# Performance work log

Hardware: AMD Instinct MI355X
Metric: run time of the kernel (lower is better)

## Reference

```python
import jax, jax.numpy as jnp
import numpy as np

B, R, NM, H, P1, G1, RC1, LAT = 16384, 360, 200, 256, 512, 256, 256, 128


def _linear_params(k, out_f, in_f):
    s = 1.0 / np.sqrt(in_f)
    kw, kb = jax.random.split(k)
    W = jax.random.uniform(kw, (out_f, in_f), minval=-s, maxval=s, dtype=jnp.float32)
    b = jax.random.uniform(kb, (out_f,), minval=-s, maxval=s, dtype=jnp.float32)
    return W, b


def setup_inputs() -> dict:
    key = jax.random.key(0)
    ks = jax.random.split(key, 14)
    x_window = jax.random.normal(ks[0], (B, 3, R), dtype=jnp.float32)
    modes = jax.random.normal(ks[1], (R, NM), dtype=jnp.float32)
    mode_coeff = jax.random.normal(ks[2], (B, NM), dtype=jnp.float32)
    W1, b1 = _linear_params(ks[3], H, 3 * R)      # surrogate layer 1
    W2, b2 = _linear_params(ks[4], H, H)          # surrogate layer 2
    W3, b3 = _linear_params(ks[5], R, H)          # surrogate layer 3
    Wp1, bp1 = _linear_params(ks[6], P1, R * R)   # npi_proj
    Wp2, bp2 = _linear_params(ks[7], LAT, P1)
    Wg1, bg1 = _linear_params(ks[8], G1, NM)      # geo_proj
    Wg2, bg2 = _linear_params(ks[9], LAT, G1)
    Wr1, br1 = _linear_params(ks[10], RC1, LAT)   # recon
    Wr2, br2 = _linear_params(ks[11], R, RC1)
    return dict(x_window=x_window, modes=modes, mode_coeff=mode_coeff,
                W1=W1, b1=b1, W2=W2, b2=b2, W3=W3, b3=b3,
                Wp1=Wp1, bp1=bp1, Wp2=Wp2, bp2=bp2,
                Wg1=Wg1, bg1=bg1, Wg2=Wg2, bg2=bg2,
                Wr1=Wr1, br1=br1, Wr2=Wr2, br2=br2)


def reference(x_window, modes, mode_coeff,
              W1, b1, W2, b2, W3, b3,
              Wp1, bp1, Wp2, bp2,
              Wg1, bg1, Wg2, bg2,
              Wr1, br1, Wr2, br2):
    Bs = x_window.shape[0]
    Rr = W3.shape[0]
    # ---- NPI surrogate forward (needed for ReLU masks) ----
    z = x_window.reshape(Bs, 3 * Rr)                       # (B, 3R)
    h1 = z @ W1.T + b1                                     # (B, H)
    m1 = (h1 > 0).astype(z.dtype)
    h2 = (h1 * m1) @ W2.T + b2                             # (B, H)
    m2 = (h2 > 0).astype(z.dtype)
    # ---- EC: exact batch-mean Jacobian of the ReLU MLP w.r.t last timestep ----
    # mean_b [ W3 diag(m2_b) W2 diag(m1_b) W1_last ] = W3 @ (W2 * (m2^T m1 / B)) @ W1[:, -R:]
    G = (m2.T @ m1) / Bs                                   # (H, H)
    ec = W3 @ ((W2 * G) @ W1[:, -Rr:])                     # (R, R); row j = dy_j/dx
    ec = jax.lax.stop_gradient(ec)                         # create_graph=False in original
    # ---- projections ----
    ec_flat = ec.reshape(1, Rr * Rr)
    z_npi1 = jax.nn.relu(ec_flat @ Wp1.T + bp1) @ Wp2.T + bp2   # (1, LAT)
    z_npi = jnp.tile(z_npi1, (Bs, 1))                           # (B, LAT)
    z_geo = jax.nn.relu(mode_coeff @ Wg1.T + bg1) @ Wg2.T + bg2  # (B, LAT)
    zsum = z_npi + z_geo
    zn = zsum / jnp.maximum(jnp.linalg.norm(zsum, axis=-1, keepdims=True), 1e-12)
    recon = jax.nn.relu(zn @ Wr1.T + br1) @ Wr2.T + br2          # (B, R)
    return (z_npi, z_geo, zn, ec, recon)
```

## Files before the change

kernel.cpp:

```cpp
#include <hip/hip_runtime.h>

typedef __bf16 bf16x8 __attribute__((ext_vector_type(8)));
typedef __bf16 bf16x4 __attribute__((ext_vector_type(4)));
typedef float  f32x4  __attribute__((ext_vector_type(4)));

__device__ __forceinline__ f32x4 mfma_bf16(bf16x8 a, bf16x8 b, f32x4 c) {
  return __builtin_amdgcn_mfma_f32_16x16x32_bf16(a, b, c, 0, 0, 0);
}
__device__ __forceinline__ bf16x8 ldB(const __bf16* Bp, int kt, int NT, int nt,
                                      int lane) {
  return *reinterpret_cast<const bf16x8*>(Bp + (((size_t)kt * NT + nt) * 64 + lane) * 8);
}

__global__ void pack_all(const float* __restrict__ W1, const float* __restrict__ W2,
                         const float* __restrict__ Wg1, const float* __restrict__ Wg2,
                         const float* __restrict__ Wr1, const float* __restrict__ Wr2,
                         __bf16* __restrict__ W1p, __bf16* __restrict__ W2p,
                         __bf16* __restrict__ Wg1p, __bf16* __restrict__ Wg2p,
                         __bf16* __restrict__ Wr1p, __bf16* __restrict__ Wr2p,
                         float* __restrict__ G) {
  int bx = blockIdx.x;
  int lane = threadIdx.x;
  if (bx >= 1104) {
    float4* g = (float4*)G;
    int base = (bx - 1104) * 512 + lane;
#pragma unroll
    for (int i = 0; i < 8; ++i) g[base + i * 64] = make_float4(0.f, 0.f, 0.f, 0.f);
    return;
  }
  const float* W; __bf16* out; int N, K, NT, local;
  if (bx < 544)      { W = W1;  out = W1p;  N = 256; K = 1080; NT = 16; local = bx; }
  else if (bx < 672) { W = W2;  out = W2p;  N = 256; K = 256;  NT = 16; local = bx - 544; }
  else if (bx < 784) { W = Wg1; out = Wg1p; N = 256; K = 200;  NT = 16; local = bx - 672; }
  else if (bx < 848) { W = Wg2; out = Wg2p; N = 128; K = 256;  NT = 8;  local = bx - 784; }
  else if (bx < 912) { W = Wr1; out = Wr1p; N = 256; K = 128;  NT = 16; local = bx - 848; }
  else               { W = Wr2; out = Wr2p; N = 360; K = 256;  NT = 24; local = bx - 912; }
  int nt = local % NT, kt = local / NT;
  int n = nt * 16 + (lane & 15);
  int k0 = kt * 32 + (lane >> 4) * 8;
  bf16x8 v;
#pragma unroll
  for (int e = 0; e < 8; ++e) {
    int k = k0 + e;
    float xv = (n < N && k < K) ? W[(size_t)n * K + k] : 0.f;
    v[e] = (__bf16)xv;
  }
  *reinterpret_cast<bf16x8*>(out + ((size_t)local * 64 + lane) * 8) = v;
}

__global__ __launch_bounds__(256) void h1h2_fused(
    const float* __restrict__ x, const __bf16* __restrict__ W1p,
    const float* __restrict__ b1, const __bf16* __restrict__ W2p,
    const float* __restrict__ b2, __bf16* __restrict__ m1T,
    __bf16* __restrict__ m2T) {
  __shared__ __bf16 Alds[32][68];
  __shared__ __bf16 h1s[32][264];
  int tid = threadIdx.x;
  int lane = tid & 63, wid = tid >> 6;
  int rowBase = blockIdx.x * 32;
  int sr = tid >> 3, sc = (tid & 7) * 8;
  const float* aSrc = x + (size_t)(rowBase + sr) * 1080;
  f32x4 acc[2][4] = {};
  float4 c0a, c0b, c1a, c1b;
  auto LD = [&](int s, float4& a, float4& b) {
    int gk = s * 64 + sc;
    if (gk < 1080) {
      a = *(const float4*)(aSrc + gk);
      b = *(const float4*)(aSrc + gk + 4);
    } else {
      a = make_float4(0.f, 0.f, 0.f, 0.f);
      b = a;
    }
  };
  LD(0, c0a, c0b);
  LD(1, c1a, c1b);
  for (int s = 0; s < 17; ++s) {
    bf16x8 w8;
    w8[0] = (__bf16)c0a.x; w8[1] = (__bf16)c0a.y; w8[2] = (__bf16)c0a.z; w8[3] = (__bf16)c0a.w;
    w8[4] = (__bf16)c0b.x; w8[5] = (__bf16)c0b.y; w8[6] = (__bf16)c0b.z; w8[7] = (__bf16)c0b.w;
    *reinterpret_cast<bf16x8*>(&Alds[sr][sc]) = w8;
    __syncthreads();
    c0a = c1a; c0b = c1b;
    if (s + 2 < 17) LD(s + 2, c1a, c1b);
    int arow = lane & 15;
#pragma unroll
    for (int ks = 0; ks < 2; ++ks) {
      int ak = ks * 32 + (lane >> 4) * 8;
      bf16x8 a0 = *reinterpret_cast<const bf16x8*>(&Alds[arow][ak]);
      bf16x8 a1 = *reinterpret_cast<const bf16x8*>(&Alds[arow + 16][ak]);
      int kt = s * 2 + ks;
#pragma unroll
      for (int n = 0; n < 4; ++n) {
        bf16x8 bv = ldB(W1p, kt, 16, wid * 4 + n, lane);
        acc[0][n] = mfma_bf16(a0, bv, acc[0][n]);
        acc[1][n] = mfma_bf16(a1, bv, acc[1][n]);
      }
    }
    __syncthreads();
  }
  int q4 = (lane >> 4) * 4;
#pragma unroll
  for (int m = 0; m < 2; ++m)
#pragma unroll
    for (int n = 0; n < 4; ++n) {
      int col = wid * 64 + n * 16 + (lane & 15);
      float bb = b1[col];
#pragma unroll
      for (int j = 0; j < 4; ++j) {
        int rl = m * 16 + q4 + j;
        float h = acc[m][n][j] + bb;
        m1T[(size_t)col * 16384 + rowBase + rl] = (__bf16)(h > 0.f ? 1.f : 0.f);
        h1s[rl][col] = (__bf16)fmaxf(h, 0.f);
      }
    }
  __syncthreads();
  f32x4 acc2[2][4] = {};
#pragma unroll
  for (int ks = 0; ks < 8; ++ks) {
    int arow = lane & 15, ak = ks * 32 + (lane >> 4) * 8;
    bf16x8 a0 = *reinterpret_cast<const bf16x8*>(&h1s[arow][ak]);
    bf16x8 a1 = *reinterpret_cast<const bf16x8*>(&h1s[arow + 16][ak]);
#pragma unroll
    for (int n = 0; n < 4; ++n) {
      bf16x8 bv = ldB(W2p, ks, 16, wid * 4 + n, lane);
      acc2[0][n] = mfma_bf16(a0, bv, acc2[0][n]);
      acc2[1][n] = mfma_bf16(a1, bv, acc2[1][n]);
    }
  }
#pragma unroll
  for (int m = 0; m < 2; ++m)
#pragma unroll
    for (int n = 0; n < 4; ++n) {
      int col = wid * 64 + n * 16 + (lane & 15);
      float bb = b2[col];
#pragma unroll
      for (int j = 0; j < 4; ++j) {
        int rl = m * 16 + q4 + j;
        float h = acc2[m][n][j] + bb;
        m2T[(size_t)col * 16384 + rowBase + rl] = (__bf16)(h > 0.f ? 1.f : 0.f);
      }
    }
}

__global__ __launch_bounds__(256) void gemm_masks(
    const __bf16* __restrict__ m2T, const __bf16* __restrict__ m1T,
    float* __restrict__ G) {
  int tid = threadIdx.x;
  int lane = tid & 63, wid = tid >> 6;
  int wr = wid >> 1, wc = wid & 1;
  int ibase = blockIdx.x * 64, jbase = blockIdx.y * 64;
  size_t b0 = (size_t)blockIdx.z * 1024 + (lane >> 4) * 8;
  const __bf16* pa0 = m2T + (size_t)(ibase + wr * 32 + (lane & 15)) * 16384 + b0;
  const __bf16* pa1 = pa0 + (size_t)16 * 16384;
  const __bf16* pb0 = m1T + (size_t)(jbase + wc * 32 + (lane & 15)) * 16384 + b0;
  const __bf16* pb1 = pb0 + (size_t)16 * 16384;
  f32x4 acc[2][2] = {};
#pragma unroll 4
  for (int c = 0; c < 32; ++c) {
    bf16x8 a0 = *reinterpret_cast<const bf16x8*>(pa0 + c * 32);
    bf16x8 a1 = *reinterpret_cast<const bf16x8*>(pa1 + c * 32);
    bf16x8 bv0 = *reinterpret_cast<const bf16x8*>(pb0 + c * 32);
    bf16x8 bv1 = *reinterpret_cast<const bf16x8*>(pb1 + c * 32);
    acc[0][0] = mfma_bf16(a0, bv0, acc[0][0]);
    acc[0][1] = mfma_bf16(a0, bv1, acc[0][1]);
    acc[1][0] = mfma_bf16(a1, bv0, acc[1][0]);
    acc[1][1] = mfma_bf16(a1, bv1, acc[1][1]);
  }
  int q4 = (lane >> 4) * 4;
#pragma unroll
  for (int m = 0; m < 2; ++m)
#pragma unroll
    for (int n = 0; n < 2; ++n)
#pragma unroll
      for (int j = 0; j < 4; ++j) {
        int gi = ibase + wr * 32 + m * 16 + q4 + j;
        int gj = jbase + wc * 32 + n * 16 + (lane & 15);
        atomicAdd(&G[(size_t)gi * 256 + gj], acc[m][n][j] * (1.f / 16384.f));
      }
}

__global__ __launch_bounds__(256) void small_gemm(
    const float* __restrict__ A, const float* __restrict__ A2, int lda,
    const float* __restrict__ Bm, int ldb, float* __restrict__ C, int ldc,
    int M, int N, int K) {
  __shared__ float As[64][17];
  __shared__ float Bs[16][65];
  int t = threadIdx.x;
  int tx = t & 15, ty = t >> 4;
  int m0 = blockIdx.y * 64, n0 = blockIdx.x * 64;
  float acc[4][4] = {};
  for (int k0 = 0; k0 < K; k0 += 16) {
#pragma unroll
    for (int i = 0; i < 4; ++i) {
      int idx = t * 4 + i;
      int r = idx >> 4, kk = idx & 15;
      int gm = m0 + r, gk = k0 + kk;
      float v = (gm < M && gk < K) ? A[(size_t)gm * lda + gk] : 0.f;
      if (A2 && gm < M && gk < K) v *= A2[(size_t)gm * lda + gk];
      As[r][kk] = v;
      int kk2 = idx >> 6, cc = idx & 63;
      int gk2 = k0 + kk2, gn = n0 + cc;
      Bs[kk2][cc] = (gk2 < K && gn < N) ? Bm[(size_t)gk2 * ldb + gn] : 0.f;
    }
    __syncthreads();
#pragma unroll
    for (int kk = 0; kk < 16; ++kk)
#pragma unroll
      for (int i = 0; i < 4; ++i)
#pragma unroll
        for (int j = 0; j < 4; ++j)
          acc[i][j] += As[ty * 4 + i][kk] * Bs[kk][tx * 4 + j];
    __syncthreads();
  }
#pragma unroll
  for (int i = 0; i < 4; ++i)
#pragma unroll
    for (int j = 0; j < 4; ++j) {
      int gm = m0 + ty * 4 + i, gn = n0 + tx * 4 + j;
      if (gm < M && gn < N) C[(size_t)gm * ldc + gn] = acc[i][j];
    }
}

__global__ __launch_bounds__(512) void p_and_g1(
    const float* __restrict__ Wp1, const float* __restrict__ ec,
    const float* __restrict__ bp1, float* __restrict__ p,
    const float* __restrict__ mc, const __bf16* __restrict__ Wg1p,
    const float* __restrict__ bg1, const __bf16* __restrict__ Wg2p,
    const float* __restrict__ bg2, float* __restrict__ o_zgeo) {
  __shared__ __bf16 Alds[64][40];
  __shared__ __bf16 g1S[64][264];
  __shared__ float redw[8];
  int t = threadIdx.x;
  if (blockIdx.x < 512) {
    int row = blockIdx.x;
    const float4* w = (const float4*)(Wp1 + (size_t)row * 129600);
    const float4* e = (const float4*)ec;
    float s = 0.f;
    for (int i = t; i < 32400; i += 512) {
      float4 a = w[i], b = e[i];
      s += a.x * b.x + a.y * b.y + a.z * b.z + a.w * b.w;
    }
    for (int o = 32; o; o >>= 1) s += __shfl_down(s, o);
    if ((t & 63) == 0) redw[t >> 6] = s;
    __syncthreads();
    if (t == 0) {
      float tot = 0.f;
#pragma unroll
      for (int i = 0; i < 8; ++i) tot += redw[i];
      p[row] = fmaxf(tot + bp1[row], 0.f);
    }
  } else {
    int lane = t & 63, wid = t >> 6;
    int wr = wid >> 2, wc = wid & 3;
    int rowBase = (blockIdx.x - 512) * 64;
    int sr = t >> 3, sc = (t & 7) * 4;
    const float* aSrc = mc + (size_t)(rowBase + sr) * 200;
    int q4 = (lane >> 4) * 4;
    f32x4 acc[2][4] = {};
    for (int kt = 0; kt < 7; ++kt) {
      int gk = kt * 32 + sc;
      bf16x4 w4;
      if (gk < 200) {
        float4 v = *(const float4*)(aSrc + gk);
        w4[0] = (__bf16)v.x; w4[1] = (__bf16)v.y;
        w4[2] = (__bf16)v.z; w4[3] = (__bf16)v.w;
      } else {
        w4[0] = w4[1] = w4[2] = w4[3] = (__bf16)0.f;
      }
      *reinterpret_cast<bf16x4*>(&Alds[sr][sc]) = w4;
      __syncthreads();
      int arow = wr * 32 + (lane & 15), ak = (lane >> 4) * 8;
      bf16x8 a0 = *reinterpret_cast<const bf16x8*>(&Alds[arow][ak]);
      bf16x8 a1 = *reinterpret_cast<const bf16x8*>(&Alds[arow + 16][ak]);
#pragma unroll
      for (int n = 0; n < 4; ++n) {
        bf16x8 bv = ldB(Wg1p, kt, 16, wc * 4 + n, lane);
        acc[0][n] = mfma_bf16(a0, bv, acc[0][n]);
        acc[1][n] = mfma_bf16(a1, bv, acc[1][n]);
      }
      __syncthreads();
    }
#pragma unroll
    for (int m = 0; m < 2; ++m)
#pragma unroll
      for (int n = 0; n < 4; ++n) {
        int col = wc * 64 + n * 16 + (lane & 15);
        float bb = bg1[col];
#pragma unroll
        for (int j = 0; j < 4; ++j) {
          int rl = wr * 32 + m * 16 + q4 + j;
          g1S[rl][col] = (__bf16)fmaxf(acc[m][n][j] + bb, 0.f);
        }
      }
    __syncthreads();
    f32x4 acc2[2][2] = {};
#pragma unroll
    for (int ks = 0; ks < 8; ++ks) {
      int arow = wr * 32 + (lane & 15), ak = ks * 32 + (lane >> 4) * 8;
      bf16x8 a0 = *reinterpret_cast<const bf16x8*>(&g1S[arow][ak]);
      bf16x8 a1 = *reinterpret_cast<const bf16x8*>(&g1S[arow + 16][ak]);
#pragma unroll
      for (int n = 0; n < 2; ++n) {
        bf16x8 bv = ldB(Wg2p, ks, 8, wc * 2 + n, lane);
        acc2[0][n] = mfma_bf16(a0, bv, acc2[0][n]);
        acc2[1][n] = mfma_bf16(a1, bv, acc2[1][n]);
      }
    }
#pragma unroll
    for (int m = 0; m < 2; ++m)
#pragma unroll
      for (int n = 0; n < 2; ++n) {
        int col = wc * 32 + n * 16 + (lane & 15);
        float bb = bg2[col];
#pragma unroll
        for (int j = 0; j < 4; ++j) {
          int row = rowBase + wr * 32 + m * 16 + q4 + j;
          o_zgeo[(size_t)row * 128 + col] = acc2[m][n][j] + bb;
        }
      }
  }
}

__global__ void gemv_z(const float* __restrict__ p, const float* __restrict__ Wp2,
                       const float* __restrict__ bp2, float* __restrict__ znpi1) {
  int j = blockIdx.x;
  int t = threadIdx.x;
  const float4* w = (const float4*)(Wp2 + (size_t)j * 512);
  const float4* pp = (const float4*)p;
  float4 a0 = w[t], b0 = pp[t];
  float4 a1 = w[t + 64], b1 = pp[t + 64];
  float s = a0.x * b0.x + a0.y * b0.y + a0.z * b0.z + a0.w * b0.w +
            a1.x * b1.x + a1.y * b1.y + a1.z * b1.z + a1.w * b1.w;
  for (int o = 32; o; o >>= 1) s += __shfl_down(s, o);
  if (t == 0) znpi1[j] = s + bp2[j];
}

__global__ __launch_bounds__(512) void mega_tail(
    const float* __restrict__ zgeo, const float* __restrict__ znpi1,
    const __bf16* __restrict__ Wr1p, const float* __restrict__ br1,
    const __bf16* __restrict__ Wr2p, const float* __restrict__ br2,
    float* __restrict__ o_znpi, float* __restrict__ o_zn,
    float* __restrict__ o_rec) {
  __shared__ __bf16 r1S[64][264];
  __shared__ __bf16 znS[64][136];
  __shared__ float znpiS[128];
  int tid = threadIdx.x;
  int lane = tid & 63, wid = tid >> 6;
  int wr = wid >> 2, wc = wid & 3;
  int rowBase = blockIdx.x * 64;
  int q4 = (lane >> 4) * 4;
  if (tid < 128) znpiS[tid] = znpi1[tid];
  __syncthreads();
  {
    int rg = tid >> 5;
    int c4 = (tid & 31) * 4;
    float4 zp = make_float4(znpiS[c4], znpiS[c4 + 1], znpiS[c4 + 2], znpiS[c4 + 3]);
#pragma unroll
    for (int ri = 0; ri < 4; ++ri) {
      int rl = rg + ri * 16;
      int row = rowBase + rl;
      float4 zg = *(const float4*)(zgeo + (size_t)row * 128 + c4);
      float4 zs = make_float4(zg.x + zp.x, zg.y + zp.y, zg.z + zp.z, zg.w + zp.w);
      *(float4*)(o_znpi + (size_t)row * 128 + c4) = zp;
      float ss = zs.x * zs.x + zs.y * zs.y + zs.z * zs.z + zs.w * zs.w;
      ss += __shfl_xor(ss, 1);
      ss += __shfl_xor(ss, 2);
      ss += __shfl_xor(ss, 4);
      ss += __shfl_xor(ss, 8);
      ss += __shfl_xor(ss, 16);
      float rn = 1.f / fmaxf(sqrtf(ss), 1e-12f);
      float4 zn = make_float4(zs.x * rn, zs.y * rn, zs.z * rn, zs.w * rn);
      *(float4*)(o_zn + (size_t)row * 128 + c4) = zn;
      bf16x4 znb;
      znb[0] = (__bf16)zn.x; znb[1] = (__bf16)zn.y;
      znb[2] = (__bf16)zn.z; znb[3] = (__bf16)zn.w;
      *reinterpret_cast<bf16x4*>(&znS[rl][c4]) = znb;
    }
  }
  __syncthreads();
  {
    f32x4 acc[2][4] = {};
#pragma unroll
    for (int ks = 0; ks < 4; ++ks) {
      int arow = wr * 32 + (lane & 15), ak = ks * 32 + (lane >> 4) * 8;
      bf16x8 a0 = *reinterpret_cast<const bf16x8*>(&znS[arow][ak]);
      bf16x8 a1 = *reinterpret_cast<const bf16x8*>(&znS[arow + 16][ak]);
#pragma unroll
      for (int n = 0; n < 4; ++n) {
        bf16x8 bv = ldB(Wr1p, ks, 16, wc * 4 + n, lane);
        acc[0][n] = mfma_bf16(a0, bv, acc[0][n]);
        acc[1][n] = mfma_bf16(a1, bv, acc[1][n]);
      }
    }
#pragma unroll
    for (int m = 0; m < 2; ++m)
#pragma unroll
      for (int n = 0; n < 4; ++n) {
        int col = wc * 64 + n * 16 + (lane & 15);
        float bb = br1[col];
#pragma unroll
        for (int j = 0; j < 4; ++j) {
          int rl = wr * 32 + m * 16 + q4 + j;
          r1S[rl][col] = (__bf16)fmaxf(acc[m][n][j] + bb, 0.f);
        }
      }
  }
  __syncthreads();
  {
    f32x4 acc[2][6] = {};
#pragma unroll
    for (int ks = 0; ks < 8; ++ks) {
      int arow = wr * 32 + (lane & 15), ak = ks * 32 + (lane >> 4) * 8;
      bf16x8 a0 = *reinterpret_cast<const bf16x8*>(&r1S[arow][ak]);
      bf16x8 a1 = *reinterpret_cast<const bf16x8*>(&r1S[arow + 16][ak]);
#pragma unroll
      for (int n = 0; n < 6; ++n) {
        bf16x8 bv = ldB(Wr2p, ks, 24, wc * 6 + n, lane);
        acc[0][n] = mfma_bf16(a0, bv, acc[0][n]);
        acc[1][n] = mfma_bf16(a1, bv, acc[1][n]);
      }
    }
#pragma unroll
    for (int m = 0; m < 2; ++m)
#pragma unroll
      for (int n = 0; n < 6; ++n) {
        int col = wc * 96 + n * 16 + (lane & 15);
        if (col < 360) {
          float bb = br2[col];
#pragma unroll
          for (int j = 0; j < 4; ++j) {
            int rl = wr * 32 + m * 16 + q4 + j;
            o_rec[(size_t)(rowBase + rl) * 360 + col] = acc[m][n][j] + bb;
          }
        }
      }
  }
}

extern "C" void kernel_launch(void* const* d_in, const int* in_sizes, int n_in,
                              void* d_out, int out_size, void* d_ws,
                              size_t ws_size, hipStream_t stream) {
  (void)in_sizes; (void)n_in; (void)out_size; (void)ws_size;
  const float* x   = (const float*)d_in[0];
  const float* mc  = (const float*)d_in[2];
  const float* W1  = (const float*)d_in[3];  const float* b1  = (const float*)d_in[4];
  const float* W2  = (const float*)d_in[5];  const float* b2  = (const float*)d_in[6];
  const float* W3  = (const float*)d_in[7];
  const float* Wp1 = (const float*)d_in[9];  const float* bp1 = (const float*)d_in[10];
  const float* Wp2 = (const float*)d_in[11]; const float* bp2 = (const float*)d_in[12];
  const float* Wg1 = (const float*)d_in[13]; const float* bg1 = (const float*)d_in[14];
  const float* Wg2 = (const float*)d_in[15]; const float* bg2 = (const float*)d_in[16];
  const float* Wr1 = (const float*)d_in[17]; const float* br1 = (const float*)d_in[18];
  const float* Wr2 = (const float*)d_in[19]; const float* br2 = (const float*)d_in[20];

  float* out = (float*)d_out;
  float* o_znpi = out;
  float* o_zgeo = out + 2097152;
  float* o_zn   = out + 4194304;
  float* o_ec   = out + 6291456;
  float* o_rec  = out + 6421056;

  char* ws = (char*)d_ws;
  __bf16* m1T   = (__bf16*)(ws + 0);
  __bf16* m2T   = (__bf16*)(ws + 8388608);
  float*  G     = (float*)(ws + 16777216);
  float*  T     = (float*)(ws + 17039360);
  float*  p512  = (float*)(ws + 17432576);
  float*  znpi1 = (float*)(ws + 17434624);
  __bf16* W1p   = (__bf16*)(ws + 17435648);
  __bf16* W2p   = W1p  + (size_t)544 * 512;
  __bf16* Wg1p  = W2p  + (size_t)128 * 512;
  __bf16* Wg2p  = Wg1p + (size_t)112 * 512;
  __bf16* Wr1p  = Wg2p + (size_t)64 * 512;
  __bf16* Wr2p  = Wr1p + (size_t)64 * 512;

  pack_all<<<1136, 64, 0, stream>>>(W1, W2, Wg1, Wg2, Wr1, Wr2,
                                    W1p, W2p, Wg1p, Wg2p, Wr1p, Wr2p, G);
  h1h2_fused<<<512, 256, 0, stream>>>(x, W1p, b1, W2p, b2, m1T, m2T);
  gemm_masks<<<dim3(4, 4, 16), 256, 0, stream>>>(m2T, m1T, G);
  small_gemm<<<dim3(6, 4), 256, 0, stream>>>(W2, G, 256, W1 + 720, 1080, T, 384,
                                             256, 360, 256);
  small_gemm<<<dim3(6, 6), 256, 0, stream>>>(W3, nullptr, 256, T, 384, o_ec, 360,
                                             360, 360, 256);
  p_and_g1<<<768, 512, 0, stream>>>(Wp1, o_ec, bp1, p512, mc, Wg1p, bg1,
                                    Wg2p, bg2, o_zgeo);
  gemv_z<<<128, 64, 0, stream>>>(p512, Wp2, bp2, znpi1);
  mega_tail<<<256, 512, 0, stream>>>(o_zgeo, znpi1, Wr1p, br1, Wr2p, br2,
                                     o_znpi, o_zn, o_rec);
}
```

Measured before the change: 245.9 us.

## Fuse the two small GEMMs with a grid barrier and fold the GEMV into the tail

The two chained small GEMMs for the Jacobian (T = (W2*G)@W1_last, then ec = W3@T) are merged into one 36-block kernel. The blocks synchronise through an atomic-counter grid barrier, and the counter is reset in pack_all. The Wp2 GEMV that produces z_npi is removed as a separate launch and recomputed redundantly in every block of mega_tail from p. This cuts two kernel launches and their gaps, in exchange for relying on all 36 blocks being co-resident and for repeating the 512x128 GEMV in all 256 tail blocks.

After: 261.2 us. +6.2%, slower.

```diff
diff --git a/kernel.cpp b/kernel.cpp
--- a/kernel.cpp
+++ b/kernel.cpp
@@ -10,6 +10,18 @@
 __device__ __forceinline__ bf16x8 ldB(const __bf16* Bp, int kt, int NT, int nt,
                                       int lane) {
   return *reinterpret_cast<const bf16x8*>(Bp + (((size_t)kt * NT + nt) * 64 + lane) * 8);
+}
+
+__device__ __forceinline__ void gridbar(int* cnt, int target) {
+  __syncthreads();
+  if (threadIdx.x == 0) {
+    __threadfence();
+    __hip_atomic_fetch_add(cnt, 1, __ATOMIC_RELEASE, __HIP_MEMORY_SCOPE_AGENT);
+    while (__hip_atomic_load(cnt, __ATOMIC_RELAXED, __HIP_MEMORY_SCOPE_AGENT) < target)
+      __builtin_amdgcn_s_sleep(4);
+    __threadfence();
+  }
+  __syncthreads();
 }
 
 __global__ void pack_all(const float* __restrict__ W1, const float* __restrict__ W2,
@@ -18,10 +30,11 @@
                          __bf16* __restrict__ W1p, __bf16* __restrict__ W2p,
                          __bf16* __restrict__ Wg1p, __bf16* __restrict__ Wg2p,
                          __bf16* __restrict__ Wr1p, __bf16* __restrict__ Wr2p,
-                         float* __restrict__ G) {
+                         float* __restrict__ G, int* __restrict__ cnt) {
   int bx = blockIdx.x;
   int lane = threadIdx.x;
   if (bx >= 1104) {
+    if (bx == 1104 && lane == 0) cnt[0] = 0;
     float4* g = (float4*)G;
     int base = (bx - 1104) * 512 + lane;
 #pragma unroll
@@ -179,15 +192,12 @@
       }
 }
 
-__global__ __launch_bounds__(256) void small_gemm(
-    const float* __restrict__ A, const float* __restrict__ A2, int lda,
-    const float* __restrict__ Bm, int ldb, float* __restrict__ C, int ldc,
-    int M, int N, int K) {
-  __shared__ float As[64][17];
-  __shared__ float Bs[16][65];
-  int t = threadIdx.x;
+__device__ void small_body(float (*As)[17], float (*Bs)[65], int t,
+                           const float* __restrict__ A, const float* __restrict__ A2,
+                           int lda, const float* __restrict__ Bm, int ldb,
+                           float* __restrict__ C, int ldc,
+                           int M, int N, int K, int m0, int n0) {
   int tx = t & 15, ty = t >> 4;
-  int m0 = blockIdx.y * 64, n0 = blockIdx.x * 64;
   float acc[4][4] = {};
   for (int k0 = 0; k0 < K; k0 += 16) {
 #pragma unroll
@@ -219,6 +229,21 @@
       int gm = m0 + ty * 4 + i, gn = n0 + tx * 4 + j;
       if (gm < M && gn < N) C[(size_t)gm * ldc + gn] = acc[i][j];
     }
+}
+
+__global__ __launch_bounds__(256) void small_pair(
+    const float* __restrict__ W2, const float* __restrict__ G,
+    const float* __restrict__ W1, const float* __restrict__ W3,
+    float* __restrict__ T, float* __restrict__ o_ec, int* __restrict__ cnt) {
+  __shared__ float As[64][17];
+  __shared__ float Bs[16][65];
+  int t = threadIdx.x, bid = blockIdx.x;
+  if (bid < 24)
+    small_body(As, Bs, t, W2, G, 256, W1 + 720, 1080, T, 384,
+               256, 360, 256, (bid / 6) * 64, (bid % 6) * 64);
+  gridbar(cnt, 36);
+  small_body(As, Bs, t, W3, nullptr, 256, T, 384, o_ec, 360,
+             360, 360, 256, (bid / 6) * 64, (bid % 6) * 64);
 }
 
 __global__ __launch_bounds__(512) void p_and_g1(
@@ -321,22 +346,9 @@
   }
 }
 
-__global__ void gemv_z(const float* __restrict__ p, const float* __restrict__ Wp2,
-                       const float* __restrict__ bp2, float* __restrict__ znpi1) {
-  int j = blockIdx.x;
-  int t = threadIdx.x;
-  const float4* w = (const float4*)(Wp2 + (size_t)j * 512);
-  const float4* pp = (const float4*)p;
-  float4 a0 = w[t], b0 = pp[t];
-  float4 a1 = w[t + 64], b1 = pp[t + 64];
-  float s = a0.x * b0.x + a0.y * b0.y + a0.z * b0.z + a0.w * b0.w +
-            a1.x * b1.x + a1.y * b1.y + a1.z * b1.z + a1.w * b1.w;
-  for (int o = 32; o; o >>= 1) s += __shfl_down(s, o);
-  if (t == 0) znpi1[j] = s + bp2[j];
-}
-
 __global__ __launch_bounds__(512) void mega_tail(
-    const float* __restrict__ zgeo, const float* __restrict__ znpi1,
+    const float* __restrict__ p, const float* __restrict__ Wp2,
+    const float* __restrict__ bp2, const float* __restrict__ zgeo,
     const __bf16* __restrict__ Wr1p, const float* __restrict__ br1,
     const __bf16* __restrict__ Wr2p, const float* __restrict__ br2,
     float* __restrict__ o_znpi, float* __restrict__ o_zn,
@@ -344,12 +356,28 @@
   __shared__ __bf16 r1S[64][264];
   __shared__ __bf16 znS[64][136];
   __shared__ float znpiS[128];
+  __shared__ float pS[512];
   int tid = threadIdx.x;
   int lane = tid & 63, wid = tid >> 6;
   int wr = wid >> 2, wc = wid & 3;
   int rowBase = blockIdx.x * 64;
   int q4 = (lane >> 4) * 4;
-  if (tid < 128) znpiS[tid] = znpi1[tid];
+  pS[tid] = p[tid];
+  __syncthreads();
+  {
+    int col = tid >> 2, q = tid & 3;
+    const float4* w = (const float4*)(Wp2 + (size_t)col * 512 + q * 128);
+    const float4* pv = (const float4*)(pS + q * 128);
+    float s = 0.f;
+#pragma unroll
+    for (int i = 0; i < 32; ++i) {
+      float4 a = w[i], b = pv[i];
+      s += a.x * b.x + a.y * b.y + a.z * b.z + a.w * b.w;
+    }
+    s += __shfl_xor(s, 1);
+    s += __shfl_xor(s, 2);
+    if (q == 0) znpiS[col] = s + bp2[col];
+  }
   __syncthreads();
   {
     int rg = tid >> 5;
@@ -466,25 +494,21 @@
   float*  G     = (float*)(ws + 16777216);
   float*  T     = (float*)(ws + 17039360);
   float*  p512  = (float*)(ws + 17432576);
-  float*  znpi1 = (float*)(ws + 17434624);
-  __bf16* W1p   = (__bf16*)(ws + 17435648);
+  __bf16* W1p   = (__bf16*)(ws + 17434624);
   __bf16* W2p   = W1p  + (size_t)544 * 512;
   __bf16* Wg1p  = W2p  + (size_t)128 * 512;
   __bf16* Wg2p  = Wg1p + (size_t)112 * 512;
   __bf16* Wr1p  = Wg2p + (size_t)64 * 512;
   __bf16* Wr2p  = Wr1p + (size_t)64 * 512;
+  int*    cnt   = (int*)(ws + 18565120);
 
   pack_all<<<1136, 64, 0, stream>>>(W1, W2, Wg1, Wg2, Wr1, Wr2,
-                                    W1p, W2p, Wg1p, Wg2p, Wr1p, Wr2p, G);
+                                    W1p, W2p, Wg1p, Wg2p, Wr1p, Wr2p, G, cnt);
   h1h2_fused<<<512, 256, 0, stream>>>(x, W1p, b1, W2p, b2, m1T, m2T);
   gemm_masks<<<dim3(4, 4, 16), 256, 0, stream>>>(m2T, m1T, G);
-  small_gemm<<<dim3(6, 4), 256, 0, stream>>>(W2, G, 256, W1 + 720, 1080, T, 384,
-                                             256, 360, 256);
-  small_gemm<<<dim3(6, 6), 256, 0, stream>>>(W3, nullptr, 256, T, 384, o_ec, 360,
-                                             360, 360, 256);
+  small_pair<<<36, 256, 0, stream>>>(W2, G, W1, W3, T, o_ec, cnt);
   p_and_g1<<<768, 512, 0, stream>>>(Wp1, o_ec, bp1, p512, mc, Wg1p, bg1,
                                     Wg2p, bg2, o_zgeo);
-  gemv_z<<<128, 64, 0, stream>>>(p512, Wp2, bp2, znpi1);
-  mega_tail<<<256, 512, 0, stream>>>(o_zgeo, znpi1, Wr1p, br1, Wr2p, br2,
-                                     o_znpi, o_zn, o_rec);
-}
+  mega_tail<<<256, 512, 0, stream>>>(p512, Wp2, bp2, o_zgeo, Wr1p, br1,
+                                     Wr2p, br2, o_znpi, o_zn, o_rec);
+}
```

## Fuse small Jacobian GEMMs with split-K and grid barrier; widen h1h2 blocks

Applied to the files above, without the earlier changes.

Replaces the two sequential small_gemm launches with one 144-block kernel. It computes T and ec with a 4-way split-K, joins the stages with a software grid barrier on an atomic counter, and finishes with a reduction pass over the partial ec buffers. This targets the poor parallelism of the 24- and 36-block launches and removes one launch. Separately, h1h2_fused moves to 512 threads, with each wave handling 16 rows instead of 32, to raise parallelism per block. The grid barrier assumes all 144 blocks are co-resident, and the split-K adds extra traffic through global partial buffers.

After: 221.6 us. -9.9%, faster.

```diff
diff --git a/kernel.cpp b/kernel.cpp
--- a/kernel.cpp
+++ b/kernel.cpp
@@ -10,6 +10,18 @@
 __device__ __forceinline__ bf16x8 ldB(const __bf16* Bp, int kt, int NT, int nt,
                                       int lane) {
   return *reinterpret_cast<const bf16x8*>(Bp + (((size_t)kt * NT + nt) * 64 + lane) * 8);
+}
+
+__device__ __forceinline__ void gridbar(int* cnt, int target) {
+  __syncthreads();
+  if (threadIdx.x == 0) {
+    __threadfence();
+    __hip_atomic_fetch_add(cnt, 1, __ATOMIC_RELEASE, __HIP_MEMORY_SCOPE_AGENT);
+    while (__hip_atomic_load(cnt, __ATOMIC_RELAXED, __HIP_MEMORY_SCOPE_AGENT) < target)
+      __builtin_amdgcn_s_sleep(4);
+    __threadfence();
+  }
+  __syncthreads();
 }
 
 __global__ void pack_all(const float* __restrict__ W1, const float* __restrict__ W2,
@@ -18,10 +30,11 @@
                          __bf16* __restrict__ W1p, __bf16* __restrict__ W2p,
                          __bf16* __restrict__ Wg1p, __bf16* __restrict__ Wg2p,
                          __bf16* __restrict__ Wr1p, __bf16* __restrict__ Wr2p,
-                         float* __restrict__ G) {
+                         float* __restrict__ G, int* __restrict__ cnt) {
   int bx = blockIdx.x;
   int lane = threadIdx.x;
   if (bx >= 1104) {
+    if (bx == 1104 && lane == 0) cnt[0] = 0;
     float4* g = (float4*)G;
     int base = (bx - 1104) * 512 + lane;
 #pragma unroll
@@ -48,7 +61,7 @@
   *reinterpret_cast<bf16x8*>(out + ((size_t)local * 64 + lane) * 8) = v;
 }
 
-__global__ __launch_bounds__(256) void h1h2_fused(
+__global__ __launch_bounds__(512) void h1h2_fused(
     const float* __restrict__ x, const __bf16* __restrict__ W1p,
     const float* __restrict__ b1, const __bf16* __restrict__ W2p,
     const float* __restrict__ b2, __bf16* __restrict__ m1T,
@@ -57,89 +70,76 @@
   __shared__ __bf16 h1s[32][264];
   int tid = threadIdx.x;
   int lane = tid & 63, wid = tid >> 6;
+  int wr = wid >> 2, wc = wid & 3;
   int rowBase = blockIdx.x * 32;
-  int sr = tid >> 3, sc = (tid & 7) * 8;
+  int sr = tid >> 4, sc = (tid & 15) * 4;
   const float* aSrc = x + (size_t)(rowBase + sr) * 1080;
-  f32x4 acc[2][4] = {};
-  float4 c0a, c0b, c1a, c1b;
-  auto LD = [&](int s, float4& a, float4& b) {
+  f32x4 acc[4] = {};
+  float4 c0, c1;
+  auto LD = [&](int s, float4& d) {
     int gk = s * 64 + sc;
-    if (gk < 1080) {
-      a = *(const float4*)(aSrc + gk);
-      b = *(const float4*)(aSrc + gk + 4);
-    } else {
-      a = make_float4(0.f, 0.f, 0.f, 0.f);
-      b = a;
-    }
+    d = (gk < 1080) ? *(const float4*)(aSrc + gk) : make_float4(0.f, 0.f, 0.f, 0.f);
   };
-  LD(0, c0a, c0b);
-  LD(1, c1a, c1b);
+  LD(0, c0);
+  LD(1, c1);
   for (int s = 0; s < 17; ++s) {
-    bf16x8 w8;
-    w8[0] = (__bf16)c0a.x; w8[1] = (__bf16)c0a.y; w8[2] = (__bf16)c0a.z; w8[3] = (__bf16)c0a.w;
-    w8[4] = (__bf16)c0b.x; w8[5] = (__bf16)c0b.y; w8[6] = (__bf16)c0b.z; w8[7] = (__bf16)c0b.w;
-    *reinterpret_cast<bf16x8*>(&Alds[sr][sc]) = w8;
+    bf16x4 w4;
+    w4[0] = (__bf16)c0.x; w4[1] = (__bf16)c0.y;
+    w4[2] = (__bf16)c0.z; w4[3] = (__bf16)c0.w;
+    *reinterpret_cast<bf16x4*>(&Alds[sr][sc]) = w4;
     __syncthreads();
-    c0a = c1a; c0b = c1b;
-    if (s + 2 < 17) LD(s + 2, c1a, c1b);
-    int arow = lane & 15;
+    c0 = c1;
+    if (s + 2 < 17) LD(s + 2, c1);
+    int arow = wr * 16 + (lane & 15);
 #pragma unroll
     for (int ks = 0; ks < 2; ++ks) {
       int ak = ks * 32 + (lane >> 4) * 8;
       bf16x8 a0 = *reinterpret_cast<const bf16x8*>(&Alds[arow][ak]);
-      bf16x8 a1 = *reinterpret_cast<const bf16x8*>(&Alds[arow + 16][ak]);
       int kt = s * 2 + ks;
 #pragma unroll
       for (int n = 0; n < 4; ++n) {
-        bf16x8 bv = ldB(W1p, kt, 16, wid * 4 + n, lane);
-        acc[0][n] = mfma_bf16(a0, bv, acc[0][n]);
-        acc[1][n] = mfma_bf16(a1, bv, acc[1][n]);
+        bf16x8 bv = ldB(W1p, kt, 16, wc * 4 + n, lane);
+        acc[n] = mfma_bf16(a0, bv, acc[n]);
       }
     }
     __syncthreads();
   }
   int q4 = (lane >> 4) * 4;
 #pragma unroll
-  for (int m = 0; m < 2; ++m)
+  for (int n = 0; n < 4; ++n) {
+    int col = wc * 64 + n * 16 + (lane & 15);
+    float bb = b1[col];
+#pragma unroll
+    for (int j = 0; j < 4; ++j) {
+      int rl = wr * 16 + q4 + j;
+      float h = acc[n][j] + bb;
+      m1T[(size_t)col * 16384 + rowBase + rl] = (__bf16)(h > 0.f ? 1.f : 0.f);
+      h1s[rl][col] = (__bf16)fmaxf(h, 0.f);
+    }
+  }
+  __syncthreads();
+  f32x4 acc2[4] = {};
+#pragma unroll
+  for (int ks = 0; ks < 8; ++ks) {
+    int arow = wr * 16 + (lane & 15), ak = ks * 32 + (lane >> 4) * 8;
+    bf16x8 a0 = *reinterpret_cast<const bf16x8*>(&h1s[arow][ak]);
 #pragma unroll
     for (int n = 0; n < 4; ++n) {
-      int col = wid * 64 + n * 16 + (lane & 15);
-      float bb = b1[col];
-#pragma unroll
-      for (int j = 0; j < 4; ++j) {
-        int rl = m * 16 + q4 + j;
-        float h = acc[m][n][j] + bb;
-        m1T[(size_t)col * 16384 + rowBase + rl] = (__bf16)(h > 0.f ? 1.f : 0.f);
-        h1s[rl][col] = (__bf16)fmaxf(h, 0.f);
-      }
-    }
-  __syncthreads();
-  f32x4 acc2[2][4] = {};
-#pragma unroll
-  for (int ks = 0; ks < 8; ++ks) {
-    int arow = lane & 15, ak = ks * 32 + (lane >> 4) * 8;
-    bf16x8 a0 = *reinterpret_cast<const bf16x8*>(&h1s[arow][ak]);
-    bf16x8 a1 = *reinterpret_cast<const bf16x8*>(&h1s[arow + 16][ak]);
-#pragma unroll
-    for (int n = 0; n < 4; ++n) {
-      bf16x8 bv = ldB(W2p, ks, 16, wid * 4 + n, lane);
-      acc2[0][n] = mfma_bf16(a0, bv, acc2[0][n]);
-      acc2[1][n] = mfma_bf16(a1, bv, acc2[1][n]);
-    }
-  }
-#pragma unroll
-  for (int m = 0; m < 2; ++m)
-#pragma unroll
-    for (int n = 0; n < 4; ++n) {
-      int col = wid * 64 + n * 16 + (lane & 15);
-      float bb = b2[col];
-#pragma unroll
-      for (int j = 0; j < 4; ++j) {
-        int rl = m * 16 + q4 + j;
-        float h = acc2[m][n][j] + bb;
-        m2T[(size_t)col * 16384 + rowBase + rl] = (__bf16)(h > 0.f ? 1.f : 0.f);
-      }
-    }
+      bf16x8 bv = ldB(W2p, ks, 16, wc * 4 + n, lane);
+      acc2[n] = mfma_bf16(a0, bv, acc2[n]);
+    }
+  }
+#pragma unroll
+  for (int n = 0; n < 4; ++n) {
+    int col = wc * 64 + n * 16 + (lane & 15);
+    float bb = b2[col];
+#pragma unroll
+    for (int j = 0; j < 4; ++j) {
+      int rl = wr * 16 + q4 + j;
+      float h = acc2[n][j] + bb;
+      m2T[(size_t)col * 16384 + rowBase + rl] = (__bf16)(h > 0.f ? 1.f : 0.f);
+    }
+  }
 }
 
 __global__ __launch_bounds__(256) void gemm_masks(
@@ -179,28 +179,32 @@
       }
 }
 
-__global__ __launch_bounds__(256) void small_gemm(
-    const float* __restrict__ A, const float* __restrict__ A2, int lda,
-    const float* __restrict__ Bm, int ldb, float* __restrict__ C, int ldc,
-    int M, int N, int K) {
-  __shared__ float As[64][17];
-  __shared__ float Bs[16][65];
-  int t = threadIdx.x;
+__device__ void small_body2(float (*As)[17], float (*Bs)[65], int t,
+                            const float* __restrict__ A, const float* __restrict__ A2,
+                            int lda, const float* __restrict__ Bm, int ldb,
+                            bool sum4, size_t bStride, float* __restrict__ C,
+                            int ldc, int M, int N, int kBeg, int kEnd,
+                            int m0, int n0) {
   int tx = t & 15, ty = t >> 4;
-  int m0 = blockIdx.y * 64, n0 = blockIdx.x * 64;
   float acc[4][4] = {};
-  for (int k0 = 0; k0 < K; k0 += 16) {
+  for (int k0 = kBeg; k0 < kEnd; k0 += 16) {
 #pragma unroll
     for (int i = 0; i < 4; ++i) {
       int idx = t * 4 + i;
       int r = idx >> 4, kk = idx & 15;
       int gm = m0 + r, gk = k0 + kk;
-      float v = (gm < M && gk < K) ? A[(size_t)gm * lda + gk] : 0.f;
-      if (A2 && gm < M && gk < K) v *= A2[(size_t)gm * lda + gk];
+      float v = (gm < M) ? A[(size_t)gm * lda + gk] : 0.f;
+      if (A2 && gm < M) v *= A2[(size_t)gm * lda + gk];
       As[r][kk] = v;
       int kk2 = idx >> 6, cc = idx & 63;
       int gk2 = k0 + kk2, gn = n0 + cc;
-      Bs[kk2][cc] = (gk2 < K && gn < N) ? Bm[(size_t)gk2 * ldb + gn] : 0.f;
+      float bv = 0.f;
+      if (gn < N) {
+        const float* bp = Bm + (size_t)gk2 * ldb + gn;
+        bv = bp[0];
+        if (sum4) bv = bv + bp[bStride] + bp[2 * bStride] + bp[3 * bStride];
+      }
+      Bs[kk2][cc] = bv;
     }
     __syncthreads();
 #pragma unroll
@@ -219,6 +223,38 @@
       int gm = m0 + ty * 4 + i, gn = n0 + tx * 4 + j;
       if (gm < M && gn < N) C[(size_t)gm * ldc + gn] = acc[i][j];
     }
+}
+
+__global__ __launch_bounds__(256) void small_split(
+    const float* __restrict__ W2, const float* __restrict__ G,
+    const float* __restrict__ W1, const float* __restrict__ W3,
+    float* __restrict__ Tpart, float* __restrict__ ecpart,
+    float* __restrict__ o_ec, int* __restrict__ cnt) {
+  __shared__ float As[64][17];
+  __shared__ float Bs[16][65];
+  int t = threadIdx.x, bid = blockIdx.x;
+  if (bid < 96) {
+    int tile = bid >> 2, kc = bid & 3;
+    small_body2(As, Bs, t, W2, G, 256, W1 + 720, 1080, false, 0,
+                Tpart + (size_t)kc * 98304, 384, 256, 360,
+                kc * 64, kc * 64 + 64, (tile / 6) * 64, (tile % 6) * 64);
+  }
+  gridbar(cnt, 144);
+  {
+    int tile = bid >> 2, kc = bid & 3;
+    small_body2(As, Bs, t, W3, nullptr, 256, Tpart, 384, true, 98304,
+                ecpart + (size_t)kc * 129600, 360, 360, 360,
+                kc * 64, kc * 64 + 64, (tile / 6) * 64, (tile % 6) * 64);
+  }
+  gridbar(cnt, 288);
+  {
+    int base = bid * 900;
+    for (int i = t; i < 900; i += 256) {
+      int idx = base + i;
+      o_ec[idx] = ecpart[idx] + ecpart[129600 + idx] + ecpart[259200 + idx] +
+                  ecpart[388800 + idx];
+    }
+  }
 }
 
 __global__ __launch_bounds__(512) void p_and_g1(
@@ -461,27 +497,26 @@
   float* o_rec  = out + 6421056;
 
   char* ws = (char*)d_ws;
-  __bf16* m1T   = (__bf16*)(ws + 0);
-  __bf16* m2T   = (__bf16*)(ws + 8388608);
-  float*  G     = (float*)(ws + 16777216);
-  float*  T     = (float*)(ws + 17039360);
-  float*  p512  = (float*)(ws + 17432576);
-  float*  znpi1 = (float*)(ws + 17434624);
-  __bf16* W1p   = (__bf16*)(ws + 17435648);
-  __bf16* W2p   = W1p  + (size_t)544 * 512;
-  __bf16* Wg1p  = W2p  + (size_t)128 * 512;
-  __bf16* Wg2p  = Wg1p + (size_t)112 * 512;
-  __bf16* Wr1p  = Wg2p + (size_t)64 * 512;
-  __bf16* Wr2p  = Wr1p + (size_t)64 * 512;
+  __bf16* m1T    = (__bf16*)(ws + 0);
+  __bf16* m2T    = (__bf16*)(ws + 8388608);
+  float*  G      = (float*)(ws + 16777216);
+  float*  Tpart  = (float*)(ws + 17039360);
+  float*  ecpart = (float*)(ws + 18612224);
+  float*  p512   = (float*)(ws + 20686848);
+  float*  znpi1  = (float*)(ws + 20688896);
+  __bf16* W1p    = (__bf16*)(ws + 20689920);
+  __bf16* W2p    = W1p  + (size_t)544 * 512;
+  __bf16* Wg1p   = W2p  + (size_t)128 * 512;
+  __bf16* Wg2p   = Wg1p + (size_t)112 * 512;
+  __bf16* Wr1p   = Wg2p + (size_t)64 * 512;
+  __bf16* Wr2p   = Wr1p + (size_t)64 * 512;
+  int*    cnt    = (int*)(ws + 22020096);
 
   pack_all<<<1136, 64, 0, stream>>>(W1, W2, Wg1, Wg2, Wr1, Wr2,
-                                    W1p, W2p, Wg1p, Wg2p, Wr1p, Wr2p, G);
-  h1h2_fused<<<512, 256, 0, stream>>>(x, W1p, b1, W2p, b2, m1T, m2T);
+                                    W1p, W2p, Wg1p, Wg2p, Wr1p, Wr2p, G, cnt);
+  h1h2_fused<<<512, 512, 0, stream>>>(x, W1p, b1, W2p, b2, m1T, m2T);
   gemm_masks<<<dim3(4, 4, 16), 256, 0, stream>>>(m2T, m1T, G);
-  small_gemm<<<dim3(6, 4), 256, 0, stream>>>(W2, G, 256, W1 + 720, 1080, T, 384,
-                                             256, 360, 256);
-  small_gemm<<<dim3(6, 6), 256, 0, stream>>>(W3, nullptr, 256, T, 384, o_ec, 360,
-                                             360, 360, 256);
+  small_split<<<144, 256, 0, stream>>>(W2, G, W1, W3, Tpart, ecpart, o_ec, cnt);
   p_and_g1<<<768, 512, 0, stream>>>(Wp1, o_ec, bp1, p512, mc, Wg1p, bg1,
                                     Wg2p, bg2, o_zgeo);
   gemv_z<<<128, 64, 0, stream>>>(p512, Wp2, bp2, znpi1);
```
